# Kernel tuning notes

Measured on AMD Instinct MI355X. Metric: run time of the kernel, lower is better.

The kernel has to match this reference:

```python
import jax, jax.numpy as jnp
import numpy as np

N_NODES, N_EDGES, N_GRAPHS = 100000, 400000, 4096
F_NODE, F_EDGE, G = 78, 11, 256
NUM_LAYERS, NUM_TIMESTEPS = 3, 2
L = NUM_LAYERS - 1  # number of GNNLayers after GetContext


def _lrelu(x):
    return jax.nn.leaky_relu(x, 0.01)


def _seg_softmax(logits, seg, n):
    # softmax of logits grouped by segment id (edge_softmax over dst / softmax_nodes over graph)
    m = jax.ops.segment_max(logits, seg, num_segments=n)
    e = jnp.exp(logits - m[seg])
    s = jax.ops.segment_sum(e, seg, num_segments=n)
    return e / s[seg]


def _gru(x, h, Wih, Whh, bih, bhh):
    gi = x @ Wih.T + bih
    gh = h @ Whh.T + bhh
    ir, iz, inn = jnp.split(gi, 3, axis=-1)
    hr, hz, hn = jnp.split(gh, 3, axis=-1)
    r = jax.nn.sigmoid(ir + hr)
    z = jax.nn.sigmoid(iz + hz)
    nn_ = jnp.tanh(inn + r * hn)
    return (1.0 - z) * nn_ + z * h


def _forward(node_feats, edge_feats, W_pn, b_pn, W_pe1, b_pe1, W_pe2, b_pe2, W_et, b_et,
             gru0_Wih, gru0_Whh, gru0_bih, gru0_bhh,
             gnn_W_pe, gnn_b_pe, gnn_W_pn, gnn_b_pn, gnn_Wih, gnn_Whh, gnn_bih, gnn_bhh,
             ro_W_cl, ro_b_cl, ro_W_pn, ro_b_pn, ro_Wih, ro_Whh, ro_bih, ro_bhh,
             ln_gamma, ln_beta, src, dst, node_graph):
    N, B = node_feats.shape[0], N_GRAPHS
    # ---- GetContext ----
    hv_new = _lrelu(node_feats @ W_pn.T + b_pn)                                  # [N,G]
    he1 = _lrelu(jnp.concatenate([node_feats[src], edge_feats], -1) @ W_pe1.T + b_pe1)  # [E,G]
    logits = _lrelu(jnp.concatenate([hv_new[dst], he1], -1) @ W_pe2.T + b_pe2)   # [E,1]
    a = _seg_softmax(logits, dst, N)
    c = jax.ops.segment_sum(a * (he1 @ W_et.T + b_et), dst, num_segments=N)      # [N,G]
    h = jax.nn.relu(_gru(jax.nn.elu(c), hv_new, gru0_Wih, gru0_Whh, gru0_bih, gru0_bhh))
    # ---- GNNLayers (AttentiveGRU2) ----
    for l in range(L):
        lg = _lrelu(jnp.concatenate([h[dst], h[src]], -1) @ gnn_W_pe[l].T + gnn_b_pe[l])  # [E,1]
        a = _seg_softmax(lg, dst, N)
        hv = h @ gnn_W_pn[l].T + gnn_b_pn[l]
        c = jax.ops.segment_sum(a * hv[src], dst, num_segments=N)
        h = jax.nn.relu(_gru(jax.nn.elu(c), h, gnn_Wih[l], gnn_Whh[l], gnn_bih[l], gnn_bhh[l]))
    # ---- AttentiveFPReadout ----
    g_feats = jax.ops.segment_sum(h, node_graph, num_segments=B)                 # [B,G]
    for t in range(NUM_TIMESTEPS):
        z = _lrelu(jnp.concatenate([jax.nn.relu(g_feats)[node_graph], h], -1) @ ro_W_cl[t].T + ro_b_cl[t])  # [N,1]
        a = _seg_softmax(z, node_graph, B)
        hv = h @ ro_W_pn[t].T + ro_b_pn[t]
        gr = jax.ops.segment_sum(a * hv, node_graph, num_segments=B)
        g_feats = jax.nn.relu(_gru(jax.nn.elu(gr), g_feats, ro_Wih[t], ro_Whh[t], ro_bih[t], ro_bhh[t]))
    # ---- LayerNorm (dropout is identity at inference) ----
    mu = jnp.mean(g_feats, -1, keepdims=True)
    var = jnp.mean((g_feats - mu) ** 2, -1, keepdims=True)
    return (g_feats - mu) / jnp.sqrt(var + 1e-5) * ln_gamma + ln_beta


def setup_inputs() -> dict:
    key = jax.random.key(0)
    ks = iter(jax.random.split(key, 64))

    def nrm(shape, scale=1.0):
        return jax.random.normal(next(ks), shape, dtype=jnp.float32) * scale

    def lin(out_d, in_d):
        return nrm((out_d, in_d), 1.0 / np.sqrt(in_d))

    d = {}
    d['node_feats'] = nrm((N_NODES, F_NODE))
    d['edge_feats'] = nrm((N_EDGES, F_EDGE))
    d['src'] = jax.random.randint(next(ks), (N_EDGES,), 0, N_NODES)
    d['dst'] = jax.random.randint(next(ks), (N_EDGES,), 0, N_NODES)
    d['node_graph'] = jnp.sort(jax.random.randint(next(ks), (N_NODES,), 0, N_GRAPHS))
    # GetContext params
    d['W_pn'] = lin(G, F_NODE); d['b_pn'] = jnp.zeros((G,), jnp.float32)
    d['W_pe1'] = lin(G, F_NODE + F_EDGE); d['b_pe1'] = jnp.zeros((G,), jnp.float32)
    d['W_pe2'] = lin(1, 2 * G); d['b_pe2'] = jnp.zeros((1,), jnp.float32)
    d['W_et'] = lin(G, G); d['b_et'] = jnp.zeros((G,), jnp.float32)
    d['gru0_Wih'] = lin(3 * G, G); d['gru0_Whh'] = lin(3 * G, G)
    d['gru0_bih'] = jnp.zeros((3 * G,), jnp.float32); d['gru0_bhh'] = jnp.zeros((3 * G,), jnp.float32)
    # stacked GNNLayer params
    s2g = 1.0 / np.sqrt(2 * G); sg = 1.0 / np.sqrt(G)
    d['gnn_W_pe'] = nrm((L, 1, 2 * G), s2g); d['gnn_b_pe'] = jnp.zeros((L, 1), jnp.float32)
    d['gnn_W_pn'] = nrm((L, G, G), sg); d['gnn_b_pn'] = jnp.zeros((L, G), jnp.float32)
    d['gnn_Wih'] = nrm((L, 3 * G, G), sg); d['gnn_Whh'] = nrm((L, 3 * G, G), sg)
    d['gnn_bih'] = jnp.zeros((L, 3 * G), jnp.float32); d['gnn_bhh'] = jnp.zeros((L, 3 * G), jnp.float32)
    # stacked readout (GlobalPool) params
    T = NUM_TIMESTEPS
    d['ro_W_cl'] = nrm((T, 1, 2 * G), s2g); d['ro_b_cl'] = jnp.zeros((T, 1), jnp.float32)
    d['ro_W_pn'] = nrm((T, G, G), sg); d['ro_b_pn'] = jnp.zeros((T, G), jnp.float32)
    d['ro_Wih'] = nrm((T, 3 * G, G), sg); d['ro_Whh'] = nrm((T, 3 * G, G), sg)
    d['ro_bih'] = jnp.zeros((T, 3 * G), jnp.float32); d['ro_bhh'] = jnp.zeros((T, 3 * G), jnp.float32)
    d['ln_gamma'] = jnp.ones((G,), jnp.float32); d['ln_beta'] = jnp.zeros((G,), jnp.float32)
    return d


def reference(node_feats, edge_feats, src, dst, node_graph, W_pn, b_pn, W_pe1, b_pe1, W_pe2, b_pe2,
              W_et, b_et, gru0_Wih, gru0_Whh, gru0_bih, gru0_bhh,
              gnn_W_pe, gnn_b_pe, gnn_W_pn, gnn_b_pn, gnn_Wih, gnn_Whh, gnn_bih, gnn_bhh,
              ro_W_cl, ro_b_cl, ro_W_pn, ro_b_pn, ro_Wih, ro_Whh, ro_bih, ro_bhh, ln_gamma, ln_beta):
    return _forward(node_feats, edge_feats, W_pn, b_pn, W_pe1, b_pe1, W_pe2, b_pe2, W_et, b_et,
                    gru0_Wih, gru0_Whh, gru0_bih, gru0_bhh,
                    gnn_W_pe, gnn_b_pe, gnn_W_pn, gnn_b_pn, gnn_Wih, gnn_Whh, gnn_bih, gnn_bhh,
                    ro_W_cl, ro_b_cl, ro_W_pn, ro_b_pn, ro_Wih, ro_Whh, ro_bih, ro_bhh,
                    ln_gamma, ln_beta, src, dst, node_graph)
```

## Files before the change

kernel.cpp:

```cpp
#include <hip/hip_runtime.h>

#define NN 100000
#define NE 400000
#define NB 4096
#define FN 78
#define FE 11
#define GD 256
#define NL 2
#define NT 2

typedef unsigned short u16;
typedef __attribute__((ext_vector_type(8))) short bf16x8;
typedef __attribute__((ext_vector_type(4))) float f32x4;

__device__ __forceinline__ float lrelu_(float x){ return x > 0.f ? x : 0.01f*x; }
__device__ __forceinline__ float elu_(float x){ return x > 0.f ? x : expf(x) - 1.f; }
__device__ __forceinline__ float sigm_(float x){ return 1.f/(1.f + expf(-x)); }

__device__ __forceinline__ float bf2f(u16 u){ return __uint_as_float(((unsigned)u) << 16); }
__device__ __forceinline__ u16 f2bf(float f){
  unsigned u = __float_as_uint(f);
  unsigned r = (u + 0x7fffu + ((u >> 16) & 1u)) >> 16;
  return (u16)r;
}

__global__ void k_zero(float* p, size_t n){
  size_t i = (size_t)blockIdx.x*blockDim.x + threadIdx.x;
  size_t st = (size_t)gridDim.x*blockDim.x;
  for (; i < n; i += st) p[i] = 0.f;
}

__global__ void k_count(const int* __restrict__ dst, int* __restrict__ cnt, int E){
  int e = blockIdx.x*256 + threadIdx.x;
  if (e < E) atomicAdd(&cnt[dst[e]], 1);
}
__global__ void k_scan1(const int* __restrict__ cnt, int* __restrict__ part,
                        int* __restrict__ btot, int n){
  __shared__ int sd[256];
  int i = blockIdx.x*256 + threadIdx.x;
  int v = (i < n) ? cnt[i] : 0;
  sd[threadIdx.x] = v; __syncthreads();
  for (int d=1; d<256; d<<=1){
    int t = (threadIdx.x >= d) ? sd[threadIdx.x-d] : 0;
    __syncthreads();
    sd[threadIdx.x] += t;
    __syncthreads();
  }
  if (i < n) part[i] = sd[threadIdx.x];
  if (threadIdx.x == 255) btot[blockIdx.x] = sd[255];
}
__global__ void k_scan2(const int* __restrict__ btot, int* __restrict__ boff, int nb){
  __shared__ int sd[512];
  int tid = threadIdx.x;
  int v = (tid < nb) ? btot[tid] : 0;
  sd[tid] = v; __syncthreads();
  for (int d=1; d<512; d<<=1){
    int t = (tid >= d) ? sd[tid-d] : 0;
    __syncthreads();
    sd[tid] += t;
    __syncthreads();
  }
  if (tid < nb) boff[tid] = sd[tid] - v;
}
__global__ void k_scan3(const int* __restrict__ part, const int* __restrict__ boff,
                        int* __restrict__ rowptr, int n){
  int i = blockIdx.x*256 + threadIdx.x;
  if (i < n) rowptr[i+1] = part[i] + boff[blockIdx.x];
  if (i == 0) rowptr[0] = 0;
}
__global__ void k_cursor(const int* __restrict__ rowptr, int* __restrict__ cursor, int n){
  int i = blockIdx.x*256 + threadIdx.x;
  if (i < n) cursor[i] = rowptr[i];
}
__global__ void k_fill(const int* __restrict__ dst, int* __restrict__ cursor,
                       int* __restrict__ order, int E){
  int e = blockIdx.x*256 + threadIdx.x;
  if (e < E){
    int pos = atomicAdd(&cursor[dst[e]], 1);
    order[pos] = e;
  }
}
__global__ void k_gpb(const int* __restrict__ ng, int* __restrict__ gpb, int N, int B){
  int b = blockIdx.x*256 + threadIdx.x;
  if (b > B) return;
  int lo = 0, hi = N;
  while (lo < hi){ int mid = (lo+hi)>>1; if (ng[mid] < b) lo = mid+1; else hi = mid; }
  gpb[b] = lo;
}

__global__ void k_pack_b(const float* __restrict__ W, u16* __restrict__ Bp, int OUT, int K){
  int t = blockIdx.x*256 + threadIdx.x;
  if (t >= OUT*K) return;
  int j = t & 7;
  int l = (t >> 3) & 63;
  int rest = t >> 9;
  int nks = K >> 5;
  int ks = rest % nks, c = rest / nks;
  int col = c*16 + (l & 15);
  int k = ks*32 + (l >> 4)*8 + j;
  Bp[t] = f2bf(W[(size_t)col*K + k]);
}

__global__ void k_pack_b96(const float* __restrict__ W, int ldw, u16* __restrict__ Bp){
  int t = blockIdx.x*256 + threadIdx.x;
  if (t >= 256*96) return;
  int j = t & 7;
  int l = (t >> 3) & 63;
  int rest = t >> 9;
  int ks = rest % 3, c = rest / 3;
  int col = c*16 + (l & 15);
  int k = ks*32 + (l >> 4)*8 + j;
  Bp[t] = (k < FN) ? f2bf(W[(size_t)col*ldw + k]) : (u16)0;
}

__global__ void k_pack_rz(const float* __restrict__ Wih, const float* __restrict__ Whh,
                          u16* __restrict__ Bp){
  int t = blockIdx.x*256 + threadIdx.x;
  int j = t & 7;
  int l = (t >> 3) & 63;
  int rest = t >> 9;
  int ks = rest & 15, c = rest >> 4;
  int srcrow = (c & 1)*256 + (c >> 1)*16 + (l & 15);
  int k = ks*32 + (l >> 4)*8 + j;
  float v = (k < 256) ? Wih[(size_t)srcrow*GD + k] : Whh[(size_t)srcrow*GD + (k - 256)];
  Bp[t] = f2bf(v);
}

__global__ void __launch_bounds__(512)
k_np2_mfma(const float* __restrict__ nf,
           const u16* __restrict__ BpA, const float* __restrict__ bA,
           const u16* __restrict__ BpB, const float* __restrict__ bB,
           u16* __restrict__ hv, u16* __restrict__ Pb, int N){
  int tid = threadIdx.x;
  int wv = __builtin_amdgcn_readfirstlane(tid >> 6);
  int lane = tid & 63;
  int m = lane & 15, kg = lane >> 4;
  int r0 = blockIdx.x*64;
  f32x4 accA[2][4], accB[2][4];
  #pragma unroll
  for (int t=0;t<2;t++)
    #pragma unroll
    for (int rt=0;rt<4;rt++){ accA[t][rt] = (f32x4)(0.f); accB[t][rt] = (f32x4)(0.f); }
  #pragma unroll
  for (int ks=0; ks<3; ks++){
    int koff = ks*32 + kg*8;
    bf16x8 a[4];
    #pragma unroll
    for (int rt=0; rt<4; rt++){
      int row = r0 + rt*16 + m;
      if (row > N-1) row = N-1;
      const float* base = nf + (size_t)row*FN;
      #pragma unroll
      for (int q=0;q<8;q++){
        int k = koff + q;
        a[rt][q] = (short)((k < FN) ? f2bf(base[k]) : (u16)0);
      }
    }
    #pragma unroll
    for (int t=0;t<2;t++){
      int c = wv*2 + t;
      bf16x8 bva = *(const bf16x8*)&BpA[(size_t)((c*3 + ks)*64 + lane)*8];
      bf16x8 bvb = *(const bf16x8*)&BpB[(size_t)((c*3 + ks)*64 + lane)*8];
      #pragma unroll
      for (int rt=0; rt<4; rt++){
        accA[t][rt] = __builtin_amdgcn_mfma_f32_16x16x32_bf16(a[rt], bva, accA[t][rt], 0, 0, 0);
        accB[t][rt] = __builtin_amdgcn_mfma_f32_16x16x32_bf16(a[rt], bvb, accB[t][rt], 0, 0, 0);
      }
    }
  }
  #pragma unroll
  for (int t=0;t<2;t++){
    int col = wv*32 + t*16 + m;
    float ba = bA[col], bb = bB[col];
    #pragma unroll
    for (int rt=0; rt<4; rt++){
      #pragma unroll
      for (int i=0;i<4;i++){
        int row = r0 + rt*16 + kg*4 + i;
        if (row < N){
          hv[(size_t)row*GD + col] = f2bf(lrelu_(accA[t][rt][i] + ba));
          Pb[(size_t)row*GD + col] = f2bf(accB[t][rt][i] + bb);
        }
      }
    }
  }
}

__global__ void k_dot2_bf16(const u16* __restrict__ rows, const float* __restrict__ wv,
                            float* __restrict__ za, float* __restrict__ zb, int N){
  int wav = threadIdx.x >> 6, lane = threadIdx.x & 63;
  int i = blockIdx.x*4 + wav;
  if (i >= N) return;
  int c0 = lane*4;
  ushort4 r4 = *(const ushort4*)&rows[(size_t)i*GD + c0];
  float4 wa = *(const float4*)&wv[c0];
  float4 wb = *(const float4*)&wv[GD + c0];
  float v0 = bf2f(r4.x), v1 = bf2f(r4.y), v2 = bf2f(r4.z), v3 = bf2f(r4.w);
  float va = v0*wa.x + v1*wa.y + v2*wa.z + v3*wa.w;
  float vb = v0*wb.x + v1*wb.y + v2*wb.z + v3*wb.w;
  #pragma unroll
  for (int off=32; off; off>>=1){ va += __shfl_down(va, off); vb += __shfl_down(vb, off); }
  if (lane == 0){ za[i] = va; zb[i] = vb; }
}

__global__ void k_dot1_bf16(const u16* __restrict__ rows, const float* __restrict__ wv,
                            float* __restrict__ z, int N){
  int wav = threadIdx.x >> 6, lane = threadIdx.x & 63;
  int i = blockIdx.x*4 + wav;
  if (i >= N) return;
  int c0 = lane*4;
  ushort4 r4 = *(const ushort4*)&rows[(size_t)i*GD + c0];
  float4 wa = *(const float4*)&wv[c0];
  float va = bf2f(r4.x)*wa.x + bf2f(r4.y)*wa.y + bf2f(r4.z)*wa.z + bf2f(r4.w)*wa.w;
  #pragma unroll
  for (int off=32; off; off>>=1) va += __shfl_down(va, off);
  if (lane == 0) z[i] = va;
}

__global__ void k_dotg_relu(const float* __restrict__ g, const float* __restrict__ wv,
                            float* __restrict__ zg, int B){
  int wav = threadIdx.x >> 6, lane = threadIdx.x & 63;
  int i = blockIdx.x*4 + wav;
  if (i >= B) return;
  int c0 = lane*4;
  float4 gv = *(const float4*)&g[(size_t)i*GD + c0];
  float4 wa = *(const float4*)&wv[c0];
  float va = fmaxf(gv.x,0.f)*wa.x + fmaxf(gv.y,0.f)*wa.y + fmaxf(gv.z,0.f)*wa.z + fmaxf(gv.w,0.f)*wa.w;
  #pragma unroll
  for (int off=32; off; off>>=1) va += __shfl_down(va, off);
  if (lane == 0) zg[i] = va;
}

__global__ void __launch_bounds__(256)
k_he1s(const u16* __restrict__ P, const float* __restrict__ za,
       const int* __restrict__ order, const int* __restrict__ src, const int* __restrict__ dst,
       const float* __restrict__ ef, const float* __restrict__ Wpe1,
       const float* __restrict__ bpe1, const float* __restrict__ Wpe2,
       const float* __restrict__ bpe2, u16* __restrict__ he1s, float* __restrict__ lg, int E){
  int wv = threadIdx.x >> 6, lane = threadIdx.x & 63;
  int jbase = (blockIdx.x*4 + wv)*8;
  if (jbase >= E) return;
  int c0 = lane*4;
  float wb0 = Wpe2[GD+c0], wb1 = Wpe2[GD+c0+1], wb2 = Wpe2[GD+c0+2], wb3 = Wpe2[GD+c0+3];
  float bp0 = bpe1[c0], bp1 = bpe1[c0+1], bp2 = bpe1[c0+2], bp3 = bpe1[c0+3];
  float wk0[FE], wk1[FE], wk2[FE], wk3[FE];
  #pragma unroll
  for (int k=0;k<FE;k++){
    wk0[k] = Wpe1[(size_t)(c0+0)*(FN+FE) + FN + k];
    wk1[k] = Wpe1[(size_t)(c0+1)*(FN+FE) + FN + k];
    wk2[k] = Wpe1[(size_t)(c0+2)*(FN+FE) + FN + k];
    wk3[k] = Wpe1[(size_t)(c0+3)*(FN+FE) + FN + k];
  }
  float b2 = bpe2[0];
  for (int jj=0; jj<8; jj++){
    int j = jbase + jj; if (j >= E) break;
    int e = order[j];
    int sn = src[e], d = dst[e];
    ushort4 p4 = *(const ushort4*)&P[(size_t)sn*GD + c0];
    const float* efp = &ef[(size_t)e*FE];
    float efv[FE];
    #pragma unroll
    for (int k=0;k<FE;k++) efv[k] = efp[k];
    float h0 = bf2f(p4.x)+bp0, h1 = bf2f(p4.y)+bp1, h2 = bf2f(p4.z)+bp2, h3 = bf2f(p4.w)+bp3;
    #pragma unroll
    for (int k=0;k<FE;k++){
      h0 += wk0[k]*efv[k]; h1 += wk1[k]*efv[k]; h2 += wk2[k]*efv[k]; h3 += wk3[k]*efv[k];
    }
    h0 = lrelu_(h0); h1 = lrelu_(h1); h2 = lrelu_(h2); h3 = lrelu_(h3);
    ushort4 o;
    o.x = f2bf(h0); o.y = f2bf(h1); o.z = f2bf(h2); o.w = f2bf(h3);
    *(ushort4*)&he1s[(size_t)j*GD + c0] = o;
    float part = h0*wb0 + h1*wb1 + h2*wb2 + h3*wb3;
    #pragma unroll
    for (int off=32; off; off>>=1) part += __shfl_down(part, off);
    if (lane == 0) lg[j] = lrelu_(part + za[d] + b2);
  }
}

__global__ void __launch_bounds__(256)
k_ctx_agg(const u16* __restrict__ he1s, const float* __restrict__ lg,
          const int* __restrict__ rowptr, u16* __restrict__ wc,
          float* __restrict__ sdeg, int N){
  int wv = threadIdx.x >> 6, lane = threadIdx.x & 63;
  int d = blockIdx.x*4 + wv;
  if (d >= N) return;
  int j0 = rowptr[d], j1 = rowptr[d+1];
  int c0 = lane*4;
  float M = -1e30f;
  for (int j=j0; j<j1; j++) M = fmaxf(M, lg[j]);
  float s = 0.f;
  float a0=0.f, a1=0.f, a2=0.f, a3=0.f;
  for (int j=j0; j<j1; j++){
    float p = __expf(lg[j] - M);
    ushort4 h4 = *(const ushort4*)&he1s[(size_t)j*GD + c0];
    s += p;
    a0 += p*bf2f(h4.x);
    a1 += p*bf2f(h4.y);
    a2 += p*bf2f(h4.z);
    a3 += p*bf2f(h4.w);
  }
  float inv = (j1 > j0) ? 1.f/s : 0.f;
  ushort4 o;
  o.x = f2bf(a0*inv); o.y = f2bf(a1*inv); o.z = f2bf(a2*inv); o.w = f2bf(a3*inv);
  *(ushort4*)&wc[(size_t)d*GD + c0] = o;
  if (lane == 0) sdeg[d] = (j1 > j0) ? 1.f : 0.f;
}

__global__ void __launch_bounds__(256)
k_ctx_fused(const u16* __restrict__ P, const float* __restrict__ za,
            const int* __restrict__ order, const int* __restrict__ rowptr,
            const int* __restrict__ src, const float* __restrict__ ef,
            const float* __restrict__ Wpe1, const float* __restrict__ bpe1,
            const float* __restrict__ Wpe2, const float* __restrict__ bpe2,
            u16* __restrict__ wc, float* __restrict__ sdeg, int N){
  int wv = threadIdx.x >> 6, lane = threadIdx.x & 63;
  int d = blockIdx.x*4 + wv;
  if (d >= N) return;
  int j0 = rowptr[d], j1 = rowptr[d+1];
  int c0 = lane*4;
  float wb0 = Wpe2[GD+c0], wb1 = Wpe2[GD+c0+1], wb2 = Wpe2[GD+c0+2], wb3 = Wpe2[GD+c0+3];
  float bp0 = bpe1[c0], bp1 = bpe1[c0+1], bp2 = bpe1[c0+2], bp3 = bpe1[c0+3];
  float wk0[FE], wk1[FE], wk2[FE], wk3[FE];
  #pragma unroll
  for (int k=0;k<FE;k++){
    wk0[k] = Wpe1[(size_t)(c0+0)*(FN+FE) + FN + k];
    wk1[k] = Wpe1[(size_t)(c0+1)*(FN+FE) + FN + k];
    wk2[k] = Wpe1[(size_t)(c0+2)*(FN+FE) + FN + k];
    wk3[k] = Wpe1[(size_t)(c0+3)*(FN+FE) + FN + k];
  }
  float zad = za[d] + bpe2[0];
  float m = -1e30f, s = 0.f;
  float a0=0.f, a1=0.f, a2=0.f, a3=0.f;
  for (int j=j0; j<j1; j++){
    int e = order[j];
    int sn = src[e];
    ushort4 p4 = *(const ushort4*)&P[(size_t)sn*GD + c0];
    const float* efp = &ef[(size_t)e*FE];
    float efv[FE];
    #pragma unroll
    for (int k=0;k<FE;k++) efv[k] = efp[k];
    float h0 = bf2f(p4.x)+bp0, h1 = bf2f(p4.y)+bp1, h2 = bf2f(p4.z)+bp2, h3 = bf2f(p4.w)+bp3;
    #pragma unroll
    for (int k=0;k<FE;k++){
      h0 += wk0[k]*efv[k]; h1 += wk1[k]*efv[k]; h2 += wk2[k]*efv[k]; h3 += wk3[k]*efv[k];
    }
    h0 = lrelu_(h0); h1 = lrelu_(h1); h2 = lrelu_(h2); h3 = lrelu_(h3);
    float part = h0*wb0 + h1*wb1 + h2*wb2 + h3*wb3;
    #pragma unroll
    for (int off=32; off; off>>=1) part += __shfl_down(part, off);
    float l = lrelu_(part + zad);
    l = __shfl(l, 0);
    float mn = fmaxf(m, l);
    float sc = __expf(m - mn);
    float p  = __expf(l - mn);
    s = s*sc + p;
    a0 = a0*sc + p*h0; a1 = a1*sc + p*h1; a2 = a2*sc + p*h2; a3 = a3*sc + p*h3;
    m = mn;
  }
  float inv = (j1 > j0) ? 1.f/s : 0.f;
  ushort4 o;
  o.x = f2bf(a0*inv); o.y = f2bf(a1*inv); o.z = f2bf(a2*inv); o.w = f2bf(a3*inv);
  *(ushort4*)&wc[(size_t)d*GD + c0] = o;
  if (lane == 0) sdeg[d] = (j1 > j0) ? 1.f : 0.f;
}

__global__ void __launch_bounds__(256)
k_gnn_fused(const u16* __restrict__ hv, const float* __restrict__ za, const float* __restrict__ zb,
            const int* __restrict__ order, const int* __restrict__ rowptr,
            const int* __restrict__ src, const float* __restrict__ bias,
            u16* __restrict__ cw, int N){
  int wv = threadIdx.x >> 6, lane = threadIdx.x & 63;
  int d = blockIdx.x*4 + wv;
  if (d >= N) return;
  int j0 = rowptr[d], j1 = rowptr[d+1];
  int c0 = lane*4;
  float zad = za[d] + bias[0];
  float M = -1e30f;
  for (int j=j0; j<j1; j++){
    int sn = src[order[j]];
    M = fmaxf(M, lrelu_(zad + zb[sn]));
  }
  float s = 0.f;
  float a0=0.f, a1=0.f, a2=0.f, a3=0.f;
  for (int j=j0; j<j1; j++){
    int e = order[j];
    int sn = src[e];
    float p = __expf(lrelu_(zad + zb[sn]) - M);
    ushort4 r4 = *(const ushort4*)&hv[(size_t)sn*GD + c0];
    s += p;
    a0 += p*bf2f(r4.x);
    a1 += p*bf2f(r4.y);
    a2 += p*bf2f(r4.z);
    a3 += p*bf2f(r4.w);
  }
  float inv = (j1 > j0) ? 1.f/s : 0.f;
  ushort4 o;
  o.x = f2bf(elu_(a0*inv)); o.y = f2bf(elu_(a1*inv));
  o.z = f2bf(elu_(a2*inv)); o.w = f2bf(elu_(a3*inv));
  *(ushort4*)&cw[(size_t)d*GD + c0] = o;
}

__global__ void __launch_bounds__(256)
k_ro_fused(const u16* __restrict__ hv, const float* __restrict__ zg, const float* __restrict__ zh,
           const int* __restrict__ gpb, const float* __restrict__ bias,
           float* __restrict__ gr, int B){
  int b = blockIdx.x, tid = threadIdx.x;
  int i0 = gpb[b], i1 = gpb[b+1];
  float zgb = zg[b] + bias[0];
  __shared__ float red[256];
  float lm = -1e30f;
  for (int i = i0 + tid; i < i1; i += 256) lm = fmaxf(lm, lrelu_(zgb + zh[i]));
  red[tid] = lm; __syncthreads();
  for (int d2=128; d2; d2>>=1){ if (tid < d2) red[tid] = fmaxf(red[tid], red[tid+d2]); __syncthreads(); }
  float M = red[0]; __syncthreads();
  float ls = 0.f;
  for (int i = i0 + tid; i < i1; i += 256) ls += __expf(lrelu_(zgb + zh[i]) - M);
  red[tid] = ls; __syncthreads();
  for (int d2=128; d2; d2>>=1){ if (tid < d2) red[tid] += red[tid+d2]; __syncthreads(); }
  float S = red[0];
  float acc = 0.f;
  for (int i = i0; i < i1; i++){
    float p = __expf(lrelu_(zgb + zh[i]) - M);
    acc += p * bf2f(hv[(size_t)i*GD + tid]);
  }
  gr[(size_t)b*GD + tid] = (i1 > i0) ? acc/S : 0.f;
}

__global__ void k_segsum_sorted(const u16* __restrict__ h, const int* __restrict__ gpb,
                                float* __restrict__ g, int B){
  int b = blockIdx.x, tid = threadIdx.x;
  int i0 = gpb[b], i1 = gpb[b+1];
  float acc = 0.f;
  for (int i = i0; i < i1; i++) acc += bf2f(h[(size_t)i*GD + tid]);
  g[(size_t)b*GD + tid] = acc;
}

__global__ void __launch_bounds__(512)
k_gru_mfma32(const u16* __restrict__ x, const u16* __restrict__ hprev,
             const u16* __restrict__ rzp, const u16* __restrict__ nip, const u16* __restrict__ nhp,
             const float* __restrict__ bih, const float* __restrict__ bhh,
             u16* __restrict__ hout, int R){
  int tid = threadIdx.x;
  int wv = __builtin_amdgcn_readfirstlane(tid >> 6);
  int lane = tid & 63;
  int m = lane & 15, kg = lane >> 4;
  int r0 = blockIdx.x*32;

  f32x4 arz[2][4], ani[2][2], anh[2][2];
  #pragma unroll
  for (int rt=0;rt<2;rt++){
    #pragma unroll
    for (int t=0;t<4;t++) arz[rt][t] = (f32x4)(0.f);
    #pragma unroll
    for (int t=0;t<2;t++){ ani[rt][t] = (f32x4)(0.f); anh[rt][t] = (f32x4)(0.f); }
  }

  #pragma unroll
  for (int ks=0; ks<8; ks++){
    int koff = ks*32 + kg*8;
    bf16x8 ax[2], ah[2];
    #pragma unroll
    for (int rt=0; rt<2; rt++){
      int row = r0 + rt*16 + m;
      ax[rt] = *(const bf16x8*)&x[(size_t)row*GD + koff];
      ah[rt] = *(const bf16x8*)&hprev[(size_t)row*GD + koff];
    }
    #pragma unroll
    for (int t=0;t<4;t++){
      int c = wv*4 + t;
      bf16x8 bx = *(const bf16x8*)&rzp[(size_t)((c*16 + ks    )*64 + lane)*8];
      bf16x8 bh = *(const bf16x8*)&rzp[(size_t)((c*16 + ks + 8)*64 + lane)*8];
      #pragma unroll
      for (int rt=0; rt<2; rt++){
        arz[rt][t] = __builtin_amdgcn_mfma_f32_16x16x32_bf16(ax[rt], bx, arz[rt][t], 0, 0, 0);
        arz[rt][t] = __builtin_amdgcn_mfma_f32_16x16x32_bf16(ah[rt], bh, arz[rt][t], 0, 0, 0);
      }
    }
    #pragma unroll
    for (int t=0;t<2;t++){
      int c = wv*2 + t;
      bf16x8 bi = *(const bf16x8*)&nip[(size_t)((c*8 + ks)*64 + lane)*8];
      bf16x8 bh = *(const bf16x8*)&nhp[(size_t)((c*8 + ks)*64 + lane)*8];
      #pragma unroll
      for (int rt=0; rt<2; rt++){
        ani[rt][t] = __builtin_amdgcn_mfma_f32_16x16x32_bf16(ax[rt], bi, ani[rt][t], 0, 0, 0);
        anh[rt][t] = __builtin_amdgcn_mfma_f32_16x16x32_bf16(ah[rt], bh, anh[rt][t], 0, 0, 0);
      }
    }
  }

  #pragma unroll
  for (int g=0; g<2; g++){
    int ch = (wv*2 + g)*16 + m;
    float brz_r = bih[ch] + bhh[ch];
    float brz_z = bih[ch+GD] + bhh[ch+GD];
    float bin   = bih[ch+2*GD];
    float bhn   = bhh[ch+2*GD];
    #pragma unroll
    for (int rt=0; rt<2; rt++){
      #pragma unroll
      for (int i=0;i<4;i++){
        int row = r0 + rt*16 + kg*4 + i;
        float rr = sigm_(arz[rt][2*g  ][i] + brz_r);
        float zz = sigm_(arz[rt][2*g+1][i] + brz_z);
        float nn = tanhf(ani[rt][g][i] + bin + rr*(anh[rt][g][i] + bhn));
        float hp = bf2f(hprev[(size_t)row*GD + ch]);
        float o = (1.f - zz)*nn + zz*hp;
        hout[(size_t)row*GD + ch] = f2bf(fmaxf(o, 0.f));
      }
    }
  }
}

template<int DO_ELU>
__global__ void __launch_bounds__(512)
k_proj_mfma64(const u16* __restrict__ X, const u16* __restrict__ Wp,
              const float* __restrict__ b, u16* __restrict__ Y, int R,
              const float* __restrict__ mask){
  int tid = threadIdx.x;
  int wv = __builtin_amdgcn_readfirstlane(tid >> 6);
  int lane = tid & 63;
  int m = lane & 15, kg = lane >> 4;
  int r0 = blockIdx.x*64;
  f32x4 acc[2][4];
  #pragma unroll
  for (int t=0;t<2;t++)
    #pragma unroll
    for (int rt=0;rt<4;rt++) acc[t][rt] = (f32x4)(0.f);
  #pragma unroll
  for (int ks=0; ks<8; ks++){
    int koff = ks*32 + kg*8;
    bf16x8 a[4];
    #pragma unroll
    for (int rt=0; rt<4; rt++){
      int row = r0 + rt*16 + m;
      if (row > R-1) row = R-1;
      a[rt] = *(const bf16x8*)&X[(size_t)row*GD + koff];
    }
    #pragma unroll
    for (int t=0;t<2;t++){
      int c = wv*2 + t;
      bf16x8 bv = *(const bf16x8*)&Wp[(size_t)((c*8 + ks)*64 + lane)*8];
      #pragma unroll
      for (int rt=0; rt<4; rt++)
        acc[t][rt] = __builtin_amdgcn_mfma_f32_16x16x32_bf16(a[rt], bv, acc[t][rt], 0, 0, 0);
    }
  }
  #pragma unroll
  for (int t=0;t<2;t++){
    int col = wv*32 + t*16 + m;
    float bb = b[col];
    #pragma unroll
    for (int rt=0; rt<4; rt++){
      #pragma unroll
      for (int i=0;i<4;i++){
        int row = r0 + rt*16 + kg*4 + i;
        if (row < R){
          float v = acc[t][rt][i] + bb;
          if (DO_ELU){
            float mk = (mask[row] > 0.f) ? 1.f : 0.f;
            v = elu_(v*mk);
          }
          Y[(size_t)row*GD + col] = f2bf(v);
        }
      }
    }
  }
}

__global__ void __launch_bounds__(256)
k_gru_mfma_f32(const float* __restrict__ x, const float* __restrict__ hprev,
               const u16* __restrict__ Wihp, const u16* __restrict__ Whhp,
               const float* __restrict__ bih, const float* __restrict__ bhh,
               float* __restrict__ hout, int R){
  int tid = threadIdx.x;
  int wave = __builtin_amdgcn_readfirstlane(tid >> 6);
  int lane = tid & 63;
  int m = lane & 15, kg = lane >> 4;
  int r0 = blockIdx.x*16;

  f32x4 agi[3][4], agh[3][4];
  #pragma unroll
  for (int g=0;g<3;g++)
    #pragma unroll
    for (int t=0;t<4;t++){ agi[g][t] = (f32x4)(0.f); agh[g][t] = (f32x4)(0.f); }

  #pragma unroll
  for (int ks=0; ks<8; ks++){
    int koff = ks*32 + kg*8;
    const float* xp = x + (size_t)(r0 + m)*GD + koff;
    float4 x0 = *(const float4*)xp;
    float4 x1 = *(const float4*)(xp+4);
    bf16x8 ax;
    ax[0]=(short)f2bf(elu_(x0.x)); ax[1]=(short)f2bf(elu_(x0.y));
    ax[2]=(short)f2bf(elu_(x0.z)); ax[3]=(short)f2bf(elu_(x0.w));
    ax[4]=(short)f2bf(elu_(x1.x)); ax[5]=(short)f2bf(elu_(x1.y));
    ax[6]=(short)f2bf(elu_(x1.z)); ax[7]=(short)f2bf(elu_(x1.w));
    const float* hr = hprev + (size_t)(r0 + m)*GD + koff;
    float4 h0 = *(const float4*)hr;
    float4 h1 = *(const float4*)(hr+4);
    bf16x8 ah;
    ah[0]=(short)f2bf(h0.x); ah[1]=(short)f2bf(h0.y); ah[2]=(short)f2bf(h0.z); ah[3]=(short)f2bf(h0.w);
    ah[4]=(short)f2bf(h1.x); ah[5]=(short)f2bf(h1.y); ah[6]=(short)f2bf(h1.z); ah[7]=(short)f2bf(h1.w);
    #pragma unroll
    for (int g=0;g<3;g++){
      #pragma unroll
      for (int t=0;t<4;t++){
        int c = g*16 + wave*4 + t;
        bf16x8 bi = *(const bf16x8*)&Wihp[(size_t)((c*8 + ks)*64 + lane)*8];
        bf16x8 bh = *(const bf16x8*)&Whhp[(size_t)((c*8 + ks)*64 + lane)*8];
        agi[g][t] = __builtin_amdgcn_mfma_f32_16x16x32_bf16(ax, bi, agi[g][t], 0, 0, 0);
        agh[g][t] = __builtin_amdgcn_mfma_f32_16x16x32_bf16(ah, bh, agh[g][t], 0, 0, 0);
      }
    }
  }
  #pragma unroll
  for (int t=0;t<4;t++){
    int col = wave*64 + t*16 + m;
    float bir = bih[col],      bhr = bhh[col];
    float biz = bih[col+GD],   bhz = bhh[col+GD];
    float bin = bih[col+2*GD], bhn = bhh[col+2*GD];
    #pragma unroll
    for (int i=0;i<4;i++){
      int row = r0 + kg*4 + i;
      float rr = sigm_(agi[0][t][i] + bir + agh[0][t][i] + bhr);
      float zz = sigm_(agi[1][t][i] + biz + agh[1][t][i] + bhz);
      float nn = tanhf(agi[2][t][i] + bin + rr*(agh[2][t][i] + bhn));
      float hp = hprev[(size_t)row*GD + col];
      float o = (1.f - zz)*nn + zz*hp;
      hout[(size_t)row*GD + col] = fmaxf(o, 0.f);
    }
  }
}

__global__ void k_layernorm(const float* __restrict__ gb, const float* __restrict__ gamma,
                            const float* __restrict__ beta, float* __restrict__ outb){
  int r = blockIdx.x, j = threadIdx.x;
  float v = gb[(size_t)r*GD + j];
  float s1 = v, s2 = v*v;
  #pragma unroll
  for (int off=32; off; off>>=1){ s1 += __shfl_down(s1, off); s2 += __shfl_down(s2, off); }
  __shared__ float r1[4], r2[4];
  int wv = j >> 6, lane = j & 63;
  if (lane == 0){ r1[wv] = s1; r2[wv] = s2; }
  __syncthreads();
  float S1 = r1[0]+r1[1]+r1[2]+r1[3];
  float S2 = r2[0]+r2[1]+r2[2]+r2[3];
  float mu = S1/(float)GD;
  float var = fmaxf(S2/(float)GD - mu*mu, 0.f);
  outb[(size_t)r*GD + j] = (v - mu)/sqrtf(var + 1e-5f)*gamma[j] + beta[j];
}

extern "C" void kernel_launch(void* const* d_in, const int* in_sizes, int n_in,
                              void* d_out, int out_size, void* d_ws, size_t ws_size,
                              hipStream_t stream){
  const float* node_feats = (const float*)d_in[0];
  const float* edge_feats = (const float*)d_in[1];
  const int*   src        = (const int*)d_in[2];
  const int*   dst        = (const int*)d_in[3];
  const int*   node_graph = (const int*)d_in[4];
  const float* W_pn   = (const float*)d_in[5];
  const float* b_pn   = (const float*)d_in[6];
  const float* W_pe1  = (const float*)d_in[7];
  const float* b_pe1  = (const float*)d_in[8];
  const float* W_pe2  = (const float*)d_in[9];
  const float* b_pe2  = (const float*)d_in[10];
  const float* W_et   = (const float*)d_in[11];
  const float* b_et   = (const float*)d_in[12];
  const float* g0_Wih = (const float*)d_in[13];
  const float* g0_Whh = (const float*)d_in[14];
  const float* g0_bih = (const float*)d_in[15];
  const float* g0_bhh = (const float*)d_in[16];
  const float* gnn_W_pe = (const float*)d_in[17];
  const float* gnn_b_pe = (const float*)d_in[18];
  const float* gnn_W_pn = (const float*)d_in[19];
  const float* gnn_b_pn = (const float*)d_in[20];
  const float* gnn_Wih  = (const float*)d_in[21];
  const float* gnn_Whh  = (const float*)d_in[22];
  const float* gnn_bih  = (const float*)d_in[23];
  const float* gnn_bhh  = (const float*)d_in[24];
  const float* ro_W_cl = (const float*)d_in[25];
  const float* ro_b_cl = (const float*)d_in[26];
  const float* ro_W_pn = (const float*)d_in[27];
  const float* ro_b_pn = (const float*)d_in[28];
  const float* ro_Wih  = (const float*)d_in[29];
  const float* ro_Whh  = (const float*)d_in[30];
  const float* ro_bih  = (const float*)d_in[31];
  const float* ro_bhh  = (const float*)d_in[32];
  const float* ln_gamma = (const float*)d_in[33];
  const float* ln_beta  = (const float*)d_in[34];
  float* outp = (float*)d_out;

  const int NBLK = (NN + 255)/256;

  char* w = (char*)d_ws;
  size_t need = 0;
  float* gbuf  = (float*)(w + need); need += (size_t)NB*GD*4;
  float* grbuf = (float*)(w + need); need += (size_t)NB*GD*4;
  float* za    = (float*)(w + need); need += (size_t)NN*4;
  float* zb    = (float*)(w + need); need += (size_t)NN*4;
  float* zg    = (float*)(w + need); need += (size_t)NB*4;
  float* sdeg  = (float*)(w + need); need += (size_t)NN*4;
  float* lg    = (float*)(w + need); need += (size_t)NE*4;
  int*   cnt    = (int*)(w + need); need += (size_t)NN*4;
  int*   rowptr = (int*)(w + need); need += (size_t)(NN+1)*4;
  int*   cursor = (int*)(w + need); need += (size_t)NN*4;
  int*   order  = (int*)(w + need); need += (size_t)NE*4;
  int*   gpb    = (int*)(w + need); need += (size_t)(NB+1)*4;
  int*   btot   = (int*)(w + need); need += (size_t)512*4;
  int*   boff   = (int*)(w + need); need += (size_t)512*4;
  u16*   hbuf = (u16*)(w + need); need += (size_t)NN*GD*2;
  u16*   htmp = (u16*)(w + need); need += (size_t)NN*GD*2;
  u16*   cwb  = (u16*)(w + need); need += (size_t)NN*GD*2;
  u16*   dbuf = (u16*)(w + need); need += (size_t)NN*GD*2;
  u16* pGruN = (u16*)(w + need); need += (size_t)3*393216*2;
  u16* pGruR = (u16*)(w + need); need += (size_t)4*196608*2;
  u16* pPn  = (u16*)(w + need); need += (size_t)4*GD*GD*2;
  u16* pEt  = (u16*)(w + need); need += (size_t)GD*GD*2;
  u16* pNp  = (u16*)(w + need); need += (size_t)2*256*96*2;
  if (ws_size < need) return;
  u16* he1s = (u16*)(w + need);
  bool use_sorted = (ws_size >= need + (size_t)NE*GD*2);
  u16* Pbuf   = hbuf;
  u16* hv_new = htmp;

  const size_t LW = 393216;
  const size_t OW = 196608;
  const size_t PW = (size_t)GD*GD;
  const size_t NPW = (size_t)256*96;
  const int G64 = (NN + 63)/64;
  const int G32 = NN/32;

  k_zero<<<64, 256, 0, stream>>>((float*)cnt, (size_t)NN);
  k_count<<<(NE+255)/256, 256, 0, stream>>>(dst, cnt, NE);
  k_scan1<<<NBLK, 256, 0, stream>>>(cnt, cnt, btot, NN);
  k_scan2<<<1, 512, 0, stream>>>(btot, boff, NBLK);
  k_scan3<<<NBLK, 256, 0, stream>>>(cnt, boff, rowptr, NN);
  k_cursor<<<NBLK, 256, 0, stream>>>(rowptr, cursor, NN);
  k_fill<<<(NE+255)/256, 256, 0, stream>>>(dst, cursor, order, NE);
  k_gpb<<<(NB+256)/256, 256, 0, stream>>>(node_graph, gpb, NN, NB);

  const float* wihs[3] = { g0_Wih, gnn_Wih, gnn_Wih + (size_t)3*GD*GD };
  const float* whhs[3] = { g0_Whh, gnn_Whh, gnn_Whh + (size_t)3*GD*GD };
  for (int l=0;l<3;l++){
    k_pack_rz<<<1024, 256, 0, stream>>>(wihs[l], whhs[l], pGruN + l*LW);
    k_pack_b<<<256, 256, 0, stream>>>(wihs[l] + (size_t)512*GD, pGruN + l*LW + 262144, 256, GD);
    k_pack_b<<<256, 256, 0, stream>>>(whhs[l] + (size_t)512*GD, pGruN + l*LW + 327680, 256, GD);
  }
  for (int t=0;t<NT;t++){
    k_pack_b<<<768, 256, 0, stream>>>(ro_Wih + (size_t)t*3*GD*GD, pGruR + (2*t)*OW, 768, GD);
    k_pack_b<<<768, 256, 0, stream>>>(ro_Whh + (size_t)t*3*GD*GD, pGruR + (2*t+1)*OW, 768, GD);
  }
  for (int l=0;l<NL;l++)
    k_pack_b<<<256, 256, 0, stream>>>(gnn_W_pn + (size_t)l*GD*GD, pPn + l*PW, GD, GD);
  for (int t=0;t<NT;t++)
    k_pack_b<<<256, 256, 0, stream>>>(ro_W_pn + (size_t)t*GD*GD, pPn + (2+t)*PW, GD, GD);
  k_pack_b<<<256, 256, 0, stream>>>(W_et, pEt, GD, GD);
  k_pack_b96<<<96, 256, 0, stream>>>(W_pn, FN, pNp);
  k_pack_b96<<<96, 256, 0, stream>>>(W_pe1, FN+FE, pNp + NPW);

  k_np2_mfma<<<G64, 512, 0, stream>>>(node_feats, pNp, b_pn, pNp + NPW, b_pe1,
                                      hv_new, Pbuf, NN);
  k_dot1_bf16<<<(NN+3)/4, 256, 0, stream>>>(hv_new, W_pe2, za, NN);
  if (use_sorted){
    k_he1s<<<NE/32, 256, 0, stream>>>(Pbuf, za, order, src, dst, edge_feats,
                                      W_pe1, b_pe1, W_pe2, b_pe2, he1s, lg, NE);
    k_ctx_agg<<<(NN+3)/4, 256, 0, stream>>>(he1s, lg, rowptr, cwb, sdeg, NN);
  } else {
    k_ctx_fused<<<(NN+3)/4, 256, 0, stream>>>(Pbuf, za, order, rowptr, src, edge_feats,
                                              W_pe1, b_pe1, W_pe2, b_pe2, cwb, sdeg, NN);
  }
  k_proj_mfma64<1><<<G64, 512, 0, stream>>>(cwb, pEt, b_et, dbuf, NN, sdeg);
  k_gru_mfma32<<<G32, 512, 0, stream>>>(dbuf, hv_new, pGruN + 0*LW, pGruN + 0*LW + 262144,
                                        pGruN + 0*LW + 327680, g0_bih, g0_bhh, hbuf, NN);

  for (int l=0; l<NL; l++){
    k_dot2_bf16<<<(NN+3)/4, 256, 0, stream>>>(hbuf, gnn_W_pe + (size_t)l*2*GD, za, zb, NN);
    k_proj_mfma64<0><<<G64, 512, 0, stream>>>(hbuf, pPn + l*PW, gnn_b_pn + (size_t)l*GD,
                                              htmp, NN, nullptr);
    k_gnn_fused<<<(NN+3)/4, 256, 0, stream>>>(htmp, za, zb, order, rowptr, src,
                                              gnn_b_pe + l, cwb, NN);
    k_gru_mfma32<<<G32, 512, 0, stream>>>(cwb, hbuf,
                                pGruN + (1+l)*LW, pGruN + (1+l)*LW + 262144, pGruN + (1+l)*LW + 327680,
                                gnn_bih + (size_t)l*3*GD, gnn_bhh + (size_t)l*3*GD, hbuf, NN);
  }

  k_segsum_sorted<<<NB, 256, 0, stream>>>(hbuf, gpb, gbuf, NB);
  for (int t=0; t<NT; t++){
    k_dotg_relu<<<(NB+3)/4, 256, 0, stream>>>(gbuf, ro_W_cl + (size_t)t*2*GD, zg, NB);
    k_dot1_bf16<<<(NN+3)/4, 256, 0, stream>>>(hbuf, ro_W_cl + (size_t)t*2*GD + GD, za, NN);
    k_proj_mfma64<0><<<G64, 512, 0, stream>>>(hbuf, pPn + (2+t)*PW, ro_b_pn + (size_t)t*GD,
                                              htmp, NN, nullptr);
    k_ro_fused<<<NB, 256, 0, stream>>>(htmp, zg, za, gpb, ro_b_cl + t, grbuf, NB);
    k_gru_mfma_f32<<<NB/16, 256, 0, stream>>>(grbuf, gbuf,
                                pGruR + (2*t)*OW, pGruR + (2*t+1)*OW,
                                ro_bih + (size_t)t*3*GD, ro_bhh + (size_t)t*3*GD, gbuf, NB);
  }
  k_layernorm<<<NB, 256, 0, stream>>>(gbuf, ln_gamma, ln_beta, outp);
}
```

Baseline: 1.966 ms.

## Recompute edge hidden features in aggregation instead of materializing he1s buffer

The sorted-edge path used to write a per-edge bf16 he1 tensor (E×256) and read it back during aggregation. Now the first kernel only computes attention logits, and the aggregation kernel recomputes he1 from the gathered projection and the edge features. This drops the large intermediate write/read and the workspace-size-dependent branch. In exchange the source-node gather and the small edge-feature matmul run twice. The GRU bias pointers are also moved into small arrays, which is only cleanup.

```diff
diff --git a/kernel.cpp b/kernel.cpp
--- a/kernel.cpp
+++ b/kernel.cpp
@@ -232,11 +232,11 @@
 }
 
 __global__ void __launch_bounds__(256)
-k_he1s(const u16* __restrict__ P, const float* __restrict__ za,
-       const int* __restrict__ order, const int* __restrict__ src, const int* __restrict__ dst,
-       const float* __restrict__ ef, const float* __restrict__ Wpe1,
-       const float* __restrict__ bpe1, const float* __restrict__ Wpe2,
-       const float* __restrict__ bpe2, u16* __restrict__ he1s, float* __restrict__ lg, int E){
+k_lg_ctx(const u16* __restrict__ P, const float* __restrict__ za,
+         const int* __restrict__ order, const int* __restrict__ src, const int* __restrict__ dst,
+         const float* __restrict__ ef, const float* __restrict__ Wpe1,
+         const float* __restrict__ bpe1, const float* __restrict__ Wpe2,
+         const float* __restrict__ bpe2, float* __restrict__ lg, int E){
   int wv = threadIdx.x >> 6, lane = threadIdx.x & 63;
   int jbase = (blockIdx.x*4 + wv)*8;
   if (jbase >= E) return;
@@ -267,9 +267,6 @@
       h0 += wk0[k]*efv[k]; h1 += wk1[k]*efv[k]; h2 += wk2[k]*efv[k]; h3 += wk3[k]*efv[k];
     }
     h0 = lrelu_(h0); h1 = lrelu_(h1); h2 = lrelu_(h2); h3 = lrelu_(h3);
-    ushort4 o;
-    o.x = f2bf(h0); o.y = f2bf(h1); o.z = f2bf(h2); o.w = f2bf(h3);
-    *(ushort4*)&he1s[(size_t)j*GD + c0] = o;
     float part = h0*wb0 + h1*wb1 + h2*wb2 + h3*wb3;
     #pragma unroll
     for (int off=32; off; off>>=1) part += __shfl_down(part, off);
@@ -278,62 +275,33 @@
 }
 
 __global__ void __launch_bounds__(256)
-k_ctx_agg(const u16* __restrict__ he1s, const float* __restrict__ lg,
-          const int* __restrict__ rowptr, u16* __restrict__ wc,
-          float* __restrict__ sdeg, int N){
+k_ctx_agg2(const u16* __restrict__ P, const int* __restrict__ order,
+           const int* __restrict__ rowptr, const int* __restrict__ src,
+           const float* __restrict__ ef, const float* __restrict__ Wpe1,
+           const float* __restrict__ bpe1, const float* __restrict__ lg,
+           u16* __restrict__ wc, float* __restrict__ sdeg, int N){
   int wv = threadIdx.x >> 6, lane = threadIdx.x & 63;
   int d = blockIdx.x*4 + wv;
   if (d >= N) return;
   int j0 = rowptr[d], j1 = rowptr[d+1];
   int c0 = lane*4;
+  float bp0 = bpe1[c0], bp1 = bpe1[c0+1], bp2 = bpe1[c0+2], bp3 = bpe1[c0+3];
+  float wk0[FE], wk1[FE], wk2[FE], wk3[FE];
+  #pragma unroll
+  for (int k=0;k<FE;k++){
+    wk0[k] = Wpe1[(size_t)(c0+0)*(FN+FE) + FN + k];
+    wk1[k] = Wpe1[(size_t)(c0+1)*(FN+FE) + FN + k];
+    wk2[k] = Wpe1[(size_t)(c0+2)*(FN+FE) + FN + k];
+    wk3[k] = Wpe1[(size_t)(c0+3)*(FN+FE) + FN + k];
+  }
   float M = -1e30f;
   for (int j=j0; j<j1; j++) M = fmaxf(M, lg[j]);
   float s = 0.f;
   float a0=0.f, a1=0.f, a2=0.f, a3=0.f;
   for (int j=j0; j<j1; j++){
-    float p = __expf(lg[j] - M);
-    ushort4 h4 = *(const ushort4*)&he1s[(size_t)j*GD + c0];
-    s += p;
-    a0 += p*bf2f(h4.x);
-    a1 += p*bf2f(h4.y);
-    a2 += p*bf2f(h4.z);
-    a3 += p*bf2f(h4.w);
-  }
-  float inv = (j1 > j0) ? 1.f/s : 0.f;
-  ushort4 o;
-  o.x = f2bf(a0*inv); o.y = f2bf(a1*inv); o.z = f2bf(a2*inv); o.w = f2bf(a3*inv);
-  *(ushort4*)&wc[(size_t)d*GD + c0] = o;
-  if (lane == 0) sdeg[d] = (j1 > j0) ? 1.f : 0.f;
-}
-
-__global__ void __launch_bounds__(256)
-k_ctx_fused(const u16* __restrict__ P, const float* __restrict__ za,
-            const int* __restrict__ order, const int* __restrict__ rowptr,
-            const int* __restrict__ src, const float* __restrict__ ef,
-            const float* __restrict__ Wpe1, const float* __restrict__ bpe1,
-            const float* __restrict__ Wpe2, const float* __restrict__ bpe2,
-            u16* __restrict__ wc, float* __restrict__ sdeg, int N){
-  int wv = threadIdx.x >> 6, lane = threadIdx.x & 63;
-  int d = blockIdx.x*4 + wv;
-  if (d >= N) return;
-  int j0 = rowptr[d], j1 = rowptr[d+1];
-  int c0 = lane*4;
-  float wb0 = Wpe2[GD+c0], wb1 = Wpe2[GD+c0+1], wb2 = Wpe2[GD+c0+2], wb3 = Wpe2[GD+c0+3];
-  float bp0 = bpe1[c0], bp1 = bpe1[c0+1], bp2 = bpe1[c0+2], bp3 = bpe1[c0+3];
-  float wk0[FE], wk1[FE], wk2[FE], wk3[FE];
-  #pragma unroll
-  for (int k=0;k<FE;k++){
-    wk0[k] = Wpe1[(size_t)(c0+0)*(FN+FE) + FN + k];
-    wk1[k] = Wpe1[(size_t)(c0+1)*(FN+FE) + FN + k];
-    wk2[k] = Wpe1[(size_t)(c0+2)*(FN+FE) + FN + k];
-    wk3[k] = Wpe1[(size_t)(c0+3)*(FN+FE) + FN + k];
-  }
-  float zad = za[d] + bpe2[0];
-  float m = -1e30f, s = 0.f;
-  float a0=0.f, a1=0.f, a2=0.f, a3=0.f;
-  for (int j=j0; j<j1; j++){
     int e = order[j];
     int sn = src[e];
+    float p = __expf(lg[j] - M);
     ushort4 p4 = *(const ushort4*)&P[(size_t)sn*GD + c0];
     const float* efp = &ef[(size_t)e*FE];
     float efv[FE];
@@ -344,18 +312,8 @@
     for (int k=0;k<FE;k++){
       h0 += wk0[k]*efv[k]; h1 += wk1[k]*efv[k]; h2 += wk2[k]*efv[k]; h3 += wk3[k]*efv[k];
     }
-    h0 = lrelu_(h0); h1 = lrelu_(h1); h2 = lrelu_(h2); h3 = lrelu_(h3);
-    float part = h0*wb0 + h1*wb1 + h2*wb2 + h3*wb3;
-    #pragma unroll
-    for (int off=32; off; off>>=1) part += __shfl_down(part, off);
-    float l = lrelu_(part + zad);
-    l = __shfl(l, 0);
-    float mn = fmaxf(m, l);
-    float sc = __expf(m - mn);
-    float p  = __expf(l - mn);
-    s = s*sc + p;
-    a0 = a0*sc + p*h0; a1 = a1*sc + p*h1; a2 = a2*sc + p*h2; a3 = a3*sc + p*h3;
-    m = mn;
+    s += p;
+    a0 += p*lrelu_(h0); a1 += p*lrelu_(h1); a2 += p*lrelu_(h2); a3 += p*lrelu_(h3);
   }
   float inv = (j1 > j0) ? 1.f/s : 0.f;
   ushort4 o;
@@ -719,8 +677,6 @@
   u16* pEt  = (u16*)(w + need); need += (size_t)GD*GD*2;
   u16* pNp  = (u16*)(w + need); need += (size_t)2*256*96*2;
   if (ws_size < need) return;
-  u16* he1s = (u16*)(w + need);
-  bool use_sorted = (ws_size >= need + (size_t)NE*GD*2);
   u16* Pbuf   = hbuf;
   u16* hv_new = htmp;
 
@@ -742,6 +698,8 @@
 
   const float* wihs[3] = { g0_Wih, gnn_Wih, gnn_Wih + (size_t)3*GD*GD };
   const float* whhs[3] = { g0_Whh, gnn_Whh, gnn_Whh + (size_t)3*GD*GD };
+  const float* bihs[3] = { g0_bih, gnn_bih, gnn_bih + (size_t)3*GD };
+  const float* bhhs[3] = { g0_bhh, gnn_bhh, gnn_bhh + (size_t)3*GD };
   for (int l=0;l<3;l++){
     k_pack_rz<<<1024, 256, 0, stream>>>(wihs[l], whhs[l], pGruN + l*LW);
     k_pack_b<<<256, 256, 0, stream>>>(wihs[l] + (size_t)512*GD, pGruN + l*LW + 262144, 256, GD);
@@ -762,14 +720,10 @@
   k_np2_mfma<<<G64, 512, 0, stream>>>(node_feats, pNp, b_pn, pNp + NPW, b_pe1,
                                       hv_new, Pbuf, NN);
   k_dot1_bf16<<<(NN+3)/4, 256, 0, stream>>>(hv_new, W_pe2, za, NN);
-  if (use_sorted){
-    k_he1s<<<NE/32, 256, 0, stream>>>(Pbuf, za, order, src, dst, edge_feats,
-                                      W_pe1, b_pe1, W_pe2, b_pe2, he1s, lg, NE);
-    k_ctx_agg<<<(NN+3)/4, 256, 0, stream>>>(he1s, lg, rowptr, cwb, sdeg, NN);
-  } else {
-    k_ctx_fused<<<(NN+3)/4, 256, 0, stream>>>(Pbuf, za, order, rowptr, src, edge_feats,
-                                              W_pe1, b_pe1, W_pe2, b_pe2, cwb, sdeg, NN);
-  }
+  k_lg_ctx<<<(NE/8+3)/4, 256, 0, stream>>>(Pbuf, za, order, src, dst, edge_feats,
+                                           W_pe1, b_pe1, W_pe2, b_pe2, lg, NE);
+  k_ctx_agg2<<<(NN+3)/4, 256, 0, stream>>>(Pbuf, order, rowptr, src, edge_feats,
+                                           W_pe1, b_pe1, lg, cwb, sdeg, NN);
   k_proj_mfma64<1><<<G64, 512, 0, stream>>>(cwb, pEt, b_et, dbuf, NN, sdeg);
   k_gru_mfma32<<<G32, 512, 0, stream>>>(dbuf, hv_new, pGruN + 0*LW, pGruN + 0*LW + 262144,
                                         pGruN + 0*LW + 327680, g0_bih, g0_bhh, hbuf, NN);
@@ -782,7 +736,7 @@
                                               gnn_b_pe + l, cwb, NN);
     k_gru_mfma32<<<G32, 512, 0, stream>>>(cwb, hbuf,
                                 pGruN + (1+l)*LW, pGruN + (1+l)*LW + 262144, pGruN + (1+l)*LW + 327680,
-                                gnn_bih + (size_t)l*3*GD, gnn_bhh + (size_t)l*3*GD, hbuf, NN);
+                                bihs[1+l], bhhs[1+l], hbuf, NN);
   }
 
   k_segsum_sorted<<<NB, 256, 0, stream>>>(hbuf, gpb, gbuf, NB);
```

Measured after the change: 2.183 ms. 1.11x slower.
